# Optimization experiments

Measured on AMD Instinct MI355X. Metric: run time of the kernel, lower is better.

## Reference

```python
import jax, jax.numpy as jnp
import numpy as np
import math

# ---- module config (mirrors init_kwargs) ----
FRAME_H, FRAME_W = 480, 640
HFOV = 79.0
CAM_H_CM = 88.0            # camera_height * 100
NUM_SEM = 16
RES = 5                    # map_resolution (cm/cell)
MAP_SIZE_CM = 4800
DSC = 4                    # global_downscaling
DU = 4                     # du_scale
VR = 100                   # vision_range (cells)
CAT_THR, EXP_THR, MAP_THR = 5.0, 1.0, 1.0
MIN_D_CM, MAX_D_CM = 50.0, 350.0
NC = 6                     # MC.NON_SEM_CHANNELS
ML = MAP_SIZE_CM // DSC // RES   # 240 local map cells
MG = MAP_SIZE_CM // RES          # 960 global map cells
ZMIN = int(-40 / RES)            # -8
ZB = int(360 / RES) - ZMIN       # 80 z bins
MIN_MAP_H = int(25 / RES - ZMIN)            # 13
MAX_MAP_H = int((CAM_H_CM + 1) / RES - ZMIN)  # 25
BC_R = 200 // RES                # been-close radius (cells)
CENTER_POSE = (ML * RES) / 200.0 # agent start at local map center (m)


def _affine_grid(theta, H, W):
    # theta: (B,2,3); align_corners=True convention
    ys = jnp.linspace(-1.0, 1.0, H)
    xs = jnp.linspace(-1.0, 1.0, W)
    xg, yg = jnp.meshgrid(xs, ys)
    base = jnp.stack([xg, yg, jnp.ones_like(xg)], -1)  # (H,W,3)
    return jnp.einsum('bij,hwj->bhwi', theta, base)    # (B,H,W,2)


def _grid_sample(img, grid):
    # bilinear, align_corners=True, zero padding (matches F.grid_sample)
    B, C, H, W = img.shape
    x = (grid[..., 0] + 1.0) * 0.5 * (W - 1)
    y = (grid[..., 1] + 1.0) * 0.5 * (H - 1)
    x0, y0 = jnp.floor(x), jnp.floor(y)
    flat = img.reshape(B, C, H * W)
    out = jnp.zeros_like(img)
    for dx in (0.0, 1.0):
        for dy in (0.0, 1.0):
            xi, yi = x0 + dx, y0 + dy
            w = (1.0 - jnp.abs(x - xi)) * (1.0 - jnp.abs(y - yi))
            ok = (xi >= 0) & (xi <= W - 1) & (yi >= 0) & (yi <= H - 1)
            idx = (jnp.clip(yi, 0, H - 1).astype(jnp.int32) * W
                   + jnp.clip(xi, 0, W - 1).astype(jnp.int32))
            g = jnp.take_along_axis(flat, jnp.broadcast_to(idx.reshape(B, 1, -1), (B, C, H * W)), axis=2)
            out = out + g.reshape(B, C, H, W) * (w * ok)[:, None]
    return out


def _splat(gx, gy, gz, feat, valid):
    # trilinear scatter-add of per-point features into (VR,VR,ZB) voxel grid
    # gx,gy,gz,valid: (B,P); feat: (B,P,F)
    B, P = gx.shape
    F = feat.shape[-1]
    ncell = VR * VR * ZB
    acc = jnp.zeros((B * ncell, F), feat.dtype)
    base = (jnp.arange(B) * ncell)[:, None]
    x0, y0, z0 = jnp.floor(gx), jnp.floor(gy), jnp.floor(gz)
    for dx in (0.0, 1.0):
        for dy in (0.0, 1.0):
            for dz in (0.0, 1.0):
                xi, yi, zi = x0 + dx, y0 + dy, z0 + dz
                w = (1.0 - jnp.abs(gx - xi)) * (1.0 - jnp.abs(gy - yi)) * (1.0 - jnp.abs(gz - zi))
                ok = valid & (xi >= 0) & (xi < VR) & (yi >= 0) & (yi < VR) & (zi >= 0) & (zi < ZB)
                cell = (yi.astype(jnp.int32) * VR + xi.astype(jnp.int32)) * ZB + zi.astype(jnp.int32)
                idx = jnp.clip(base + cell, 0, B * ncell - 1).reshape(-1)
                upd = (feat * (w * ok.astype(feat.dtype))[..., None]).reshape(B * P, F)
                acc = acc.at[idx].add(upd)
    return acc.reshape(B, VR, VR, ZB, F).transpose(0, 4, 1, 2, 3)  # (B,F,VR,VR,ZB)


def _forward(seq_obs, seq_pose_delta, seq_camera_poses, init_local_map,
             init_global_map, init_local_pose, init_global_pose,
             init_lmb, init_origins, seq_dones, seq_update_global):
    B, T = seq_obs.shape[:2]
    C = NUM_SEM
    f = FRAME_W / (2.0 * math.tan(math.radians(HFOV) / 2.0))
    cx, cy = FRAME_W / 2.0, FRAME_H / 2.0
    xs = ((jnp.arange(0, FRAME_W, DU) - cx) / f).astype(jnp.float32)   # (Ws,)
    zr = ((cy - jnp.arange(0, FRAME_H, DU)) / f).astype(jnp.float32)   # (Hs,)
    # camera tilt (elevation) from extrinsics (identity -> 0)
    elev = jnp.arctan2(seq_camera_poses[:, 2, 1], seq_camera_poses[:, 2, 2])
    ce, se = jnp.cos(elev)[:, None, None], jnp.sin(elev)[:, None, None]
    Hs, Ws = FRAME_H // DU, FRAME_W // DU
    P = Hs * Ws
    row = jnp.arange(ML, dtype=jnp.float32)

    def step(carry, inp):
        local_map, global_map, pose = carry
        obs, pd, done, upd = inp
        done = done.astype(bool)
        upd = upd.astype(bool)
        # episode reset
        local_map = jnp.where(done[:, None, None, None], 0.0, local_map)
        global_map = jnp.where(done[:, None, None, None], 0.0, global_map)
        pose = jnp.where(done[:, None], jnp.array([CENTER_POSE, CENTER_POSE, 0.0], jnp.float32), pose)
        # pose update (get_new_pose_batch, degrees)
        tr = jnp.radians(pose[:, 2])
        nx = pose[:, 0] + pd[:, 0] * jnp.cos(tr) - pd[:, 1] * jnp.sin(tr)
        ny = pose[:, 1] + pd[:, 0] * jnp.sin(tr) + pd[:, 1] * jnp.cos(tr)
        nt = jnp.mod(pose[:, 2] + jnp.degrees(pd[:, 2]) + 180.0, 360.0) - 180.0
        pose = jnp.stack([nx, ny, nt], -1)
        # ---- depth -> egocentric point cloud (cm) ----
        d = obs[:, 3, ::DU, ::DU]                           # (B,Hs,Ws)
        valid = (d >= MIN_D_CM) & (d <= MAX_D_CM)
        lat = d * xs[None, None, :]
        up = d * zr[None, :, None]
        fwd = d * ce + up * se
        hgt = -d * se + up * ce + CAM_H_CM
        gx = (lat / RES + VR / 2.0).reshape(B, P)
        gy = (fwd / RES).reshape(B, P)
        gz = (hgt / RES - ZMIN).reshape(B, P)
        # features: occupancy + avg-pooled semantics (du_scale pooling)
        sem = obs[:, 4:].reshape(B, C, Hs, DU, Ws, DU).mean((3, 5))
        feat = jnp.concatenate([jnp.ones((B, 1, Hs, Ws), obs.dtype), sem], 1)
        feat = feat.reshape(B, 1 + C, P).transpose(0, 2, 1)  # (B,P,F)
        vox = _splat(gx, gy, gz, feat, valid.reshape(B, P))  # (B,F,VR,VR,ZB)
        agent_hp = vox[..., MIN_MAP_H:MAX_MAP_H].sum(-1)
        all_hp = vox.sum(-1)
        fp_map = jnp.clip(agent_hp[:, 0:1] / MAP_THR, 0.0, 1.0)
        fp_exp = jnp.clip(all_hp[:, 0:1] / EXP_THR, 0.0, 1.0)
        sem_pred = jnp.clip(agent_hp[:, 1:] / CAT_THR, 0.0, 1.0)
        agent_view = jnp.zeros((B, NC + C, ML, ML), obs.dtype)
        y1, x1 = ML // 2, ML // 2 - VR // 2
        agent_view = agent_view.at[:, 0:1, y1:y1 + VR, x1:x1 + VR].set(fp_map)
        agent_view = agent_view.at[:, 1:2, y1:y1 + VR, x1:x1 + VR].set(fp_exp)
        agent_view = agent_view.at[:, NC:, y1:y1 + VR, x1:x1 + VR].set(sem_pred)
        # ---- pose transform: rotation then translation grid_sample ----
        th = jnp.radians(90.0 - pose[:, 2])
        stx = -(pose[:, 0] * 100.0 / RES - ML / 2.0) / (ML / 2.0)
        sty = -(pose[:, 1] * 100.0 / RES - ML / 2.0) / (ML / 2.0)
        c, s = jnp.cos(th), jnp.sin(th)
        z0 = jnp.zeros_like(th)
        o1 = jnp.ones_like(th)
        th_rot = jnp.stack([jnp.stack([c, -s, z0], -1), jnp.stack([s, c, z0], -1)], 1)
        th_tr = jnp.stack([jnp.stack([o1, z0, stx], -1), jnp.stack([z0, o1, sty], -1)], 1)
        warped = _grid_sample(_grid_sample(agent_view, _affine_grid(th_rot, ML, ML)),
                              _affine_grid(th_tr, ML, ML))
        # dilate obstacle channel (3x3 ones kernel, 1 iter)
        obst = jax.lax.reduce_window(warped[:, 0:1], -jnp.inf, jax.lax.max,
                                     (1, 1, 3, 3), (1, 1, 1, 1), 'SAME')
        warped = warped.at[:, 0:1].set(obst)
        local_map = jnp.maximum(local_map, warped)
        # current location / visited / been-close disks
        acx, acy = pose[:, 0] * 100.0 / RES, pose[:, 1] * 100.0 / RES
        d2 = ((row[None, None, :] - acx[:, None, None]) ** 2
              + (row[None, :, None] - acy[:, None, None]) ** 2)
        curr = (d2 <= 4.0).astype(local_map.dtype)
        local_map = local_map.at[:, 2].set(curr)
        local_map = local_map.at[:, 3].max(curr)
        local_map = local_map.at[:, 4].max((d2 <= float(BC_R ** 2)).astype(local_map.dtype))
        # global map update at local map boundaries
        gnew = jax.vmap(lambda g, l, lm: jax.lax.dynamic_update_slice(g, l, (0, lm[0], lm[2])))(
            global_map, local_map, init_lmb)
        global_map = jnp.where(upd[:, None, None, None], gnew, global_map)
        gpose = pose + init_origins
        # map features: local NC ch + maxpooled global NC ch + local sem ch
        gmax = global_map[:, :NC].reshape(B, NC, MG // DSC, DSC, MG // DSC, DSC).max((3, 5))
        mf = jnp.concatenate([local_map[:, :NC], gmax, local_map[:, NC:]], 1)
        return (local_map, global_map, pose), (mf, pose, gpose)

    xs_t = (jnp.swapaxes(seq_obs, 0, 1), jnp.swapaxes(seq_pose_delta, 0, 1),
            jnp.swapaxes(seq_dones, 0, 1), jnp.swapaxes(seq_update_global, 0, 1))
    (fl, fg, _), (mfs, lps, gps) = jax.lax.scan(
        step, (init_local_map, init_global_map, init_local_pose), xs_t)
    seq_mf = jnp.swapaxes(mfs, 0, 1)
    seq_lp = jnp.swapaxes(lps, 0, 1)
    seq_gp = jnp.swapaxes(gps, 0, 1)
    seq_lmb = jnp.broadcast_to(init_lmb[:, None], (B, T, 4))
    seq_org = jnp.broadcast_to(init_origins[:, None], (B, T, 3))
    return seq_mf, fl, fg, seq_lp, seq_gp, seq_lmb, seq_org


def setup_inputs():
    key = jax.random.key(0)
    k0, k1 = jax.random.split(key)
    B, T = 4, 4
    obs = jax.random.uniform(k0, (B, T, 4 + NUM_SEM, FRAME_H, FRAME_W), jnp.float32)
    obs = obs.at[:, :, 3].set(MIN_D_CM + obs[:, :, 3] * (MAX_D_CM - MIN_D_CM))  # depth in cm
    obs = obs.at[:, :, 4:].set((obs[:, :, 4:] > 0.9).astype(jnp.float32))       # binary seg masks
    pd = jax.random.normal(k1, (B, T, 3), jnp.float32) * jnp.array([0.25, 0.05, 0.1], jnp.float32)
    lo = (MG - ML) // 2
    lmb = jnp.tile(jnp.array([[lo, lo + ML, lo, lo + ML]], jnp.int32), (B, 1))
    origins = jnp.concatenate([jnp.full((B, 2), lo * RES / 100.0, jnp.float32),
                               jnp.zeros((B, 1), jnp.float32)], 1)
    lp = jnp.concatenate([jnp.full((B, 2), CENTER_POSE, jnp.float32),
                          jnp.zeros((B, 1), jnp.float32)], 1)
    return {
        "seq_obs": obs,
        "seq_pose_delta": pd,
        "seq_camera_poses": jnp.broadcast_to(jnp.eye(4, dtype=jnp.float32), (B, 4, 4)),
        "init_local_map": jnp.zeros((B, NC + NUM_SEM, ML, ML), jnp.float32),
        "init_global_map": jnp.zeros((B, NC + NUM_SEM, MG, MG), jnp.float32),
        "init_local_pose": lp,
        "init_global_pose": lp + origins,
        "init_origins": origins,
        "seq_dones": jnp.zeros((B, T), jnp.int32),
        "seq_update_global": jnp.ones((B, T), jnp.int32),
        "init_lmb": lmb,
    }


def reference(seq_obs, seq_pose_delta, seq_camera_poses, init_local_map, init_global_map,
              init_local_pose, init_global_pose, init_origins, seq_dones,
              seq_update_global, init_lmb):
    return _forward(seq_obs, seq_pose_delta, seq_camera_poses, init_local_map,
                    init_global_map, init_local_pose, init_global_pose,
                    init_lmb, init_origins, seq_dones, seq_update_global)
```

## Files before the change

kernel.cpp:

```cpp
#include <hip/hip_runtime.h>
#include <math.h>

#ifndef M_PI
#define M_PI 3.14159265358979323846
#endif

#define BB 4
#define TT 4
#define NSEM 16
#define CHL 22
#define CHMF 28
#define ML 240
#define MG 960
#define VR 100
#define HS 120
#define WSW 160
#define NPL 18
#define CPAD 24
#define MLSQ (ML*ML)
#define MGSQ (MG*MG)
#define VRSQ (VR*VR)
#define PPT (HS*WSW)
#define NPART 12
#define PR 9
#define NGRP 5
#define NSPLAT (BB*TT*NPART*NGRP)

#define SZ_MF (BB*TT*CHMF*MLSQ)
#define SZ_FL (BB*CHL*MLSQ)
#define SZ_FG (BB*CHL*MGSQ)
#define OFF_FL SZ_MF
#define OFF_FG (OFF_FL + SZ_FL)
#define OFF_LP (OFF_FG + SZ_FG)
#define OFF_GP (OFF_LP + BB*TT*3)
#define OFF_LMB (OFF_GP + BB*TT*3)
#define OFF_ORG (OFF_LMB + BB*TT*4)

#define WS_SCAL 0
#define WS_FLAGS (WS_SCAL + BB*TT*8)
#define WS_CACHE (WS_FLAGS + 4*BB)
#define WS_PLANES (WS_CACHE + BB*6*MLSQ)
#define WS_I2 (WS_PLANES + BB*TT*VRSQ*CPAD)
#define PTSN (BB*TT*PPT)
#define WS_GY (WS_I2 + BB*TT*NPL*MLSQ)
#define WS_GX (WS_GY + PTSN)
#define WS_WZA (WS_GX + PTSN)
#define WS_WZL (WS_WZA + PTSN)
#define WS_SEMDS (WS_WZL + PTSN)

__device__ __forceinline__ void fginit_block(const float* __restrict__ igm,
                                             const int* __restrict__ dones,
                                             const int* __restrict__ updg,
                                             const int* __restrict__ lmb,
                                             float* __restrict__ fg,
                                             float* __restrict__ out,
                                             float* __restrict__ ws,
                                             int b, int c, int idx)
{
    int i = idx / ML, j = idx % ML;
    int lastDone = -1, lastUpd = -1;
    #pragma unroll
    for (int t = 0; t < TT; t++) {
        if (dones[b*TT+t]) lastDone = t;
        if (updg[b*TT+t])  lastUpd  = t;
    }
    bool anyDone = lastDone >= 0;
    bool zeroWin = lastUpd < lastDone;
    int y0 = lmb[b*4+0], x0 = lmb[b*4+2];
    int iy0 = y0 >> 2, ix0 = x0 >> 2;
    bool inWin = (i >= iy0) && (i < iy0 + ML/4) && (j >= ix0) && (j < ix0 + ML/4);

    size_t base = ((size_t)b*CHL + c)*MGSQ + (size_t)(4*i)*MG + 4*j;
    const float* g = igm + base;
    float* go = fg + base;

    int act;
    if (inWin) act = zeroWin ? 1 : ((lastUpd >= 0) ? 2 : (anyDone ? 1 : 0));
    else       act = anyDone ? 1 : 0;

    if (c < 6) {
        float m = -3.0e38f;
        #pragma unroll
        for (int r = 0; r < 4; r++) {
            float4 q = *(const float4*)(g + (size_t)r*MG);
            if (act == 0) *(float4*)(go + (size_t)r*MG) = q;
            else if (act == 1) *(float4*)(go + (size_t)r*MG) = make_float4(0,0,0,0);
            m = fmaxf(m, fmaxf(fmaxf(q.x, q.y), fmaxf(q.z, q.w)));
        }
        ws[WS_CACHE + ((size_t)b*6 + c)*MLSQ + idx] = m;
        if (!inWin) {
            float v = m;
            for (int t = 0; t < TT; t++) {
                if (dones[b*TT+t]) v = 0.0f;
                out[(size_t)(b*TT+t)*CHMF*MLSQ + (6+c)*MLSQ + idx] = v;
            }
        }
    } else {
        if (act == 2) return;
        if (act == 1) {
            float4 z = make_float4(0,0,0,0);
            #pragma unroll
            for (int r = 0; r < 4; r++) *(float4*)(go + (size_t)r*MG) = z;
        } else {
            #pragma unroll
            for (int r = 0; r < 4; r++)
                *(float4*)(go + (size_t)r*MG) = *(const float4*)(g + (size_t)r*MG);
        }
    }
}

__global__ __launch_bounds__(256) void k_node1(const float* __restrict__ obs,
                                               const float* __restrict__ cam,
                                               const float* __restrict__ pd,
                                               const float* __restrict__ ilp,
                                               const float* __restrict__ org,
                                               const int* __restrict__ lmb,
                                               const int* __restrict__ dones,
                                               const int* __restrict__ updg,
                                               const float* __restrict__ igm,
                                               float* __restrict__ fg,
                                               float* __restrict__ out,
                                               float* __restrict__ ws)
{
    if (blockIdx.x == 0) {
        int i = threadIdx.x;
        if (i < BB*TT) {
            int b = i / TT, t = i % TT;
            for (int k = 0; k < 4; k++) out[OFF_LMB + (b*TT+t)*4 + k] = (float)lmb[b*4+k];
            for (int k = 0; k < 3; k++) out[OFF_ORG + (b*TT+t)*3 + k] = org[b*3+k];
        }
        if (i >= BB) return;
        int b = i;
        float p0 = ilp[b*3+0], p1 = ilp[b*3+1], p2 = ilp[b*3+2];
        const float D2R = 0.017453292519943295f;
        int lastDone = -1, lastUpd = -1;
        for (int t = 0; t < TT; t++) {
            if (dones[b*TT+t]) { p0 = 6.0f; p1 = 6.0f; p2 = 0.0f; lastDone = t; }
            if (updg[b*TT+t]) lastUpd = t;
            float tr = p2 * D2R;
            float c0 = cosf(tr), s0 = sinf(tr);
            float q0 = pd[(b*TT+t)*3+0], q1 = pd[(b*TT+t)*3+1], q2 = pd[(b*TT+t)*3+2];
            float nx = p0 + q0*c0 - q1*s0;
            float ny = p1 + q0*s0 + q1*c0;
            float a  = p2 + q2*57.29577951308232f + 180.0f;
            float m  = fmodf(a, 360.0f); if (m < 0.0f) m += 360.0f;
            float nt = m - 180.0f;
            p0 = nx; p1 = ny; p2 = nt;
            out[OFF_LP + (b*TT+t)*3+0] = nx;
            out[OFF_LP + (b*TT+t)*3+1] = ny;
            out[OFF_LP + (b*TT+t)*3+2] = nt;
            out[OFF_GP + (b*TT+t)*3+0] = nx + org[b*3+0];
            out[OFF_GP + (b*TT+t)*3+1] = ny + org[b*3+1];
            out[OFF_GP + (b*TT+t)*3+2] = nt + org[b*3+2];
            float th = (90.0f - nt) * D2R;
            float ax = nx*100.0f/5.0f, ay = ny*100.0f/5.0f;
            float* sc = ws + WS_SCAL + (b*TT+t)*8;
            sc[0] = cosf(th);
            sc[1] = sinf(th);
            sc[2] = -(ax - 120.0f)/120.0f;
            sc[3] = -(ay - 120.0f)/120.0f;
            sc[4] = ax;
            sc[5] = ay;
        }
        ws[WS_FLAGS + b*4 + 0] = (lastDone >= 0) ? 1.0f : 0.0f;
        ws[WS_FLAGS + b*4 + 1] = (lastUpd < lastDone) ? 1.0f : 0.0f;
        ws[WS_FLAGS + b*4 + 2] = (float)lastUpd;
        return;
    }
    if (blockIdx.x <= 75*BB*TT) {
        int bb = blockIdx.x - 1;
        int bt = bb / 75;
        int b = bt / TT;
        int p = (bb % 75)*256 + threadIdx.x;
        int h = p / WSW, w = p % WSW;
        size_t pi = (size_t)bt*PPT + p;
        const float* ob = obs + (size_t)bt * 20 * 480 * 640;
        float d = ob[(size_t)(3*480 + 4*h)*640 + 4*w];
        if (!(d >= 50.0f && d <= 350.0f)) { ws[WS_GY + pi] = -1000.0f; return; }

        double fd = 640.0 / (2.0 * tan((79.0 * M_PI / 180.0) * 0.5));
        float ff  = (float)fd;
        float xsv = (float)(4*w - 320) / ff;
        float zrv = (240.0f - (float)(4*h)) / ff;
        float elev = atan2f(cam[b*16+9], cam[b*16+10]);
        float ce = cosf(elev), se = sinf(elev);
        float up  = d * zrv;
        float fwd = d*ce + up*se;
        float hgt = -d*se + up*ce + 88.0f;
        float gx = (d*xsv)/5.0f + 50.0f;
        float gy = fwd/5.0f;
        float gz = hgt/5.0f + 8.0f;

        float z0 = floorf(gz);
        float wza = 0.0f, wzl = 0.0f;
        #pragma unroll
        for (int dz = 0; dz < 2; dz++) {
            float zi = z0 + dz;
            float wz = 1.0f - fabsf(gz - zi);
            if (zi >= 0.0f && zi < 80.0f) {
                wzl += wz;
                if (zi >= 13.0f && zi < 25.0f) wza += wz;
            }
        }
        if (wzl == 0.0f && wza == 0.0f) { ws[WS_GY + pi] = -1000.0f; return; }

        ws[WS_GY + pi]  = gy;
        ws[WS_GX + pi]  = gx;
        ws[WS_WZA + pi] = wza;
        ws[WS_WZL + pi] = wzl;

        if (wza > 0.0f) {
            const float* sb = ob + (size_t)4*480*640 + (size_t)(4*h)*640 + 4*w;
            float* so = ws + WS_SEMDS + (size_t)bt*NSEM*PPT + p;
            #pragma unroll
            for (int k = 0; k < NSEM; k++) {
                float s = 0.0f;
                #pragma unroll
                for (int r = 0; r < 4; r++) {
                    const float4 v = *(const float4*)(sb + (size_t)k*480*640 + r*640);
                    s += v.x + v.y + v.z + v.w;
                }
                so[(size_t)k*PPT] = s * 0.0625f;
            }
        }
        return;
    }
    int fb = blockIdx.x - (1 + 75*BB*TT);
    int idx = (fb % 225)*256 + threadIdx.x;
    int c = (fb / 225) % 6;
    int b = fb / (225*6);
    fginit_block(igm, dones, updg, lmb, fg, out, ws, b, c, idx);
}

__global__ __launch_bounds__(256) void k_node2(const float* __restrict__ igm,
                                               const int* __restrict__ dones,
                                               const int* __restrict__ updg,
                                               const int* __restrict__ lmb,
                                               float* __restrict__ planes,
                                               float* __restrict__ fg,
                                               float* __restrict__ out,
                                               float* __restrict__ ws)
{
    __shared__ float acc[4*PR*VR];
    int bid = blockIdx.x;
    if (bid < NSPLAT) {
        int bt = bid & 15;
        int part = (bid >> 4) % NPART;
        int grp = bid / (16*NPART);
        int rlo = part * PR;
        int c0  = (grp == 0) ? 0 : (2 + 4*(grp-1));
        int nch = (grp == 0) ? 2 : 4;
        for (int e = threadIdx.x; e < nch*PR*VR; e += 256) acc[e] = 0.0f;
        __syncthreads();

        const float* gyA  = ws + WS_GY  + (size_t)bt*PPT;
        const float* gxA  = ws + WS_GX  + (size_t)bt*PPT;
        const float* wzaA = ws + WS_WZA + (size_t)bt*PPT;
        const float* wzlA = ws + WS_WZL + (size_t)bt*PPT;
        const float* semA = ws + WS_SEMDS + (size_t)bt*NSEM*PPT + (size_t)(c0-2)*PPT;

        for (int p = threadIdx.x; p < PPT; p += 256) {
            float gy = gyA[p];
            float y0 = floorf(gy);
            if (y0 > (float)(rlo + PR - 1) || y0 + 1.0f < (float)rlo) continue;
            float wza = wzaA[p];
            if (grp != 0 && wza <= 0.0f) continue;
            float gx  = gxA[p];
            float x0 = floorf(gx);
            float sem[4];
            if (grp != 0) {
                #pragma unroll
                for (int k = 0; k < 4; k++) sem[k] = semA[(size_t)k*PPT + p];
            }
            float wzl = (grp == 0) ? wzlA[p] : 0.0f;
            #pragma unroll
            for (int dy = 0; dy < 2; dy++) {
                float yi = y0 + dy;
                if (!(yi >= 0.0f && yi < 100.0f)) continue;
                int r = (int)yi - rlo;
                if (r < 0 || r >= PR) continue;
                float wy = 1.0f - fabsf(gy - yi);
                #pragma unroll
                for (int dx = 0; dx < 2; dx++) {
                    float xi = x0 + dx;
                    if (!(xi >= 0.0f && xi < 100.0f)) continue;
                    float wxy = (1.0f - fabsf(gx - xi)) * wy;
                    if (wxy <= 0.0f) continue;
                    int cell = r*VR + (int)xi;
                    if (grp == 0) {
                        if (wza > 0.0f) atomicAdd(&acc[cell], wza*wxy);
                        if (wzl > 0.0f) atomicAdd(&acc[PR*VR + cell], wzl*wxy);
                    } else {
                        #pragma unroll
                        for (int k = 0; k < 4; k++) {
                            float sv = sem[k];
                            if (sv != 0.0f) atomicAdd(&acc[k*PR*VR + cell], sv*wza*wxy);
                        }
                    }
                }
            }
        }
        __syncthreads();

        int nrows = 100 - rlo; if (nrows > PR) nrows = PR;
        if (nrows <= 0) return;
        float* pl = planes + (size_t)bt*VRSQ*CPAD;
        for (int e = threadIdx.x; e < nch*nrows*VR; e += 256) {
            int c = e / (nrows*VR);
            int rc = e % (nrows*VR);
            int r = rc / VR, x = rc % VR;
            pl[(size_t)((rlo + r)*VR + x)*CPAD + (c0 + c)] = acc[c*PR*VR + r*VR + x];
        }
        return;
    }
    int fb = bid - NSPLAT;
    int idx = (fb % 225)*256 + threadIdx.x;
    int c = 6 + (fb / 225) % 8;
    int b = fb / (225*8);
    fginit_block(igm, dones, updg, lmb, fg, out, ws, b, c, idx);
}

__global__ __launch_bounds__(256) void k_node3(const float* __restrict__ planes,
                                               const float* __restrict__ igm,
                                               const int* __restrict__ dones,
                                               const int* __restrict__ updg,
                                               const int* __restrict__ lmb,
                                               float* __restrict__ I2,
                                               float* __restrict__ fg,
                                               float* __restrict__ out,
                                               float* __restrict__ ws)
{
    int bid = blockIdx.x;
    if (bid < 3600) {
        int bt = bid / 225;
        int idx = (bid % 225)*256 + threadIdx.x;
        int i = idx / ML, j = idx % ML;
        const float* sc = ws + WS_SCAL + bt*8;
        float c = sc[0], s = sc[1], stx = sc[2], sty = sc[3];
        float* o = I2 + (size_t)bt*NPL*MLSQ + idx;
        const float* pl = planes + (size_t)bt*VRSQ*CPAD;

        int   soff[16];
        float sw[16];
        float wsum = 0.0f;
        {
            float xg = (float)j * (float)(2.0/239.0) - 1.0f + stx;
            float yg = (float)i * (float)(2.0/239.0) - 1.0f + sty;
            float x = (xg + 1.0f)*0.5f*239.0f;
            float y = (yg + 1.0f)*0.5f*239.0f;
            float x0 = floorf(x), y0 = floorf(y);
            #pragma unroll
            for (int dy = 0; dy < 2; dy++) {
                float yi = y0 + dy;
                bool vy = (yi >= 0.0f && yi <= 239.0f);
                float wy = 1.0f - fabsf(y - yi);
                #pragma unroll
                for (int dx = 0; dx < 2; dx++) {
                    float xi = x0 + dx;
                    bool vx = (xi >= 0.0f && xi <= 239.0f);
                    float w2v = (vy && vx) ? (1.0f - fabsf(x - xi)) * wy : 0.0f;
                    int ci = (dy*2 + dx)*4;
                    float xg1 = (float)(int)xi * (float)(2.0/239.0) - 1.0f;
                    float yg1 = (float)(int)yi * (float)(2.0/239.0) - 1.0f;
                    float gxr = c*xg1 - s*yg1;
                    float gyr = s*xg1 + c*yg1;
                    float xx = (gxr + 1.0f)*0.5f*239.0f;
                    float yy = (gyr + 1.0f)*0.5f*239.0f;
                    float xx0 = floorf(xx), yy0 = floorf(yy);
                    #pragma unroll
                    for (int dy1 = 0; dy1 < 2; dy1++) {
                        float syi = yy0 + dy1;
                        bool v1y = (syi >= 120.0f && syi < 220.0f);
                        float wy1 = 1.0f - fabsf(yy - syi);
                        #pragma unroll
                        for (int dx1 = 0; dx1 < 2; dx1++) {
                            float sxi = xx0 + dx1;
                            bool v1 = v1y && (sxi >= 70.0f && sxi < 170.0f);
                            float w1v = v1 ? (1.0f - fabsf(xx - sxi)) * wy1 : 0.0f;
                            float wt = w2v * w1v;
                            soff[ci + dy1*2 + dx1] = v1 ? ((int)syi - 120)*VR + ((int)sxi - 70) : 0;
                            sw[ci + dy1*2 + dx1] = wt;
                            wsum += wt;
                        }
                    }
                }
            }
        }

        if (wsum <= 0.0f) {
            #pragma unroll
            for (int cc = 0; cc < NPL; cc++) o[(size_t)cc*MLSQ] = 0.0f;
            return;
        }
        float acc[NPL];
        #pragma unroll
        for (int cc = 0; cc < NPL; cc++) acc[cc] = 0.0f;
        #pragma unroll
        for (int k = 0; k < 16; k++) {
            float w = sw[k];
            if (w == 0.0f) continue;
            const float* pb = pl + (size_t)soff[k]*CPAD;
            float4 a0 = *(const float4*)(pb + 0);
            float4 a1 = *(const float4*)(pb + 4);
            float4 a2 = *(const float4*)(pb + 8);
            float4 a3 = *(const float4*)(pb + 12);
            float2 a4 = *(const float2*)(pb + 16);
            acc[0]  += fminf(a0.x, 1.0f) * w;
            acc[1]  += fminf(a0.y, 1.0f) * w;
            acc[2]  += fminf(a0.z / 5.0f, 1.0f) * w;
            acc[3]  += fminf(a0.w / 5.0f, 1.0f) * w;
            acc[4]  += fminf(a1.x / 5.0f, 1.0f) * w;
            acc[5]  += fminf(a1.y / 5.0f, 1.0f) * w;
            acc[6]  += fminf(a1.z / 5.0f, 1.0f) * w;
            acc[7]  += fminf(a1.w / 5.0f, 1.0f) * w;
            acc[8]  += fminf(a2.x / 5.0f, 1.0f) * w;
            acc[9]  += fminf(a2.y / 5.0f, 1.0f) * w;
            acc[10] += fminf(a2.z / 5.0f, 1.0f) * w;
            acc[11] += fminf(a2.w / 5.0f, 1.0f) * w;
            acc[12] += fminf(a3.x / 5.0f, 1.0f) * w;
            acc[13] += fminf(a3.y / 5.0f, 1.0f) * w;
            acc[14] += fminf(a3.z / 5.0f, 1.0f) * w;
            acc[15] += fminf(a3.w / 5.0f, 1.0f) * w;
            acc[16] += fminf(a4.x / 5.0f, 1.0f) * w;
            acc[17] += fminf(a4.y / 5.0f, 1.0f) * w;
        }
        #pragma unroll
        for (int cc = 0; cc < NPL; cc++) o[(size_t)cc*MLSQ] = acc[cc];
        return;
    }
    int fb = bid - 3600;
    int idx = (fb % 225)*256 + threadIdx.x;
    int c = 14 + (fb / 225) % 8;
    int b = fb / (225*8);
    fginit_block(igm, dones, updg, lmb, fg, out, ws, b, c, idx);
}

__global__ __launch_bounds__(256) void k_updl7(const float* __restrict__ I2,
                                               const float* __restrict__ ws,
                                               const float* __restrict__ ilm,
                                               const int* __restrict__ dones,
                                               const int* __restrict__ updg,
                                               const int* __restrict__ lmb,
                                               float* __restrict__ fl,
                                               float* __restrict__ fg,
                                               float* __restrict__ out)
{
    int bz = blockIdx.z;
    int b = bz / 7, g = bz % 7;
    int gi = blockIdx.y;
    int bx = blockIdx.x;
    int lane = threadIdx.x & 63, wv = threadIdx.x >> 6;
    int j0 = (bx < 3) ? bx*64 : 176;
    int j = j0 + lane;
    int i = gi*4 + wv;
    int idx = i*ML + j;

    int ncl, cl[4];
    switch (g) {
        case 0:  ncl = 1; cl[0] = 0; cl[1] = 0; cl[2] = 0; cl[3] = 0; break;
        case 1:  ncl = 3; cl[0] = 1; cl[1] = 2; cl[2] = 3; cl[3] = 0; break;
        case 2:  ncl = 2; cl[0] = 4; cl[1] = 5; cl[2] = 0; cl[3] = 0; break;
        default: ncl = 4; { int cc0 = 6 + (g-3)*4;
                 cl[0] = cc0; cl[1] = cc0+1; cl[2] = cc0+2; cl[3] = cc0+3; } break;
    }
    bool hasG = (g <= 2);

    __shared__ float red[4][3][16];

    const float* lmsrc = ilm + (size_t)b*CHL*MLSQ;
    float* lm = fl + (size_t)b*CHL*MLSQ;
    int y0 = lmb[b*4+0], x0 = lmb[b*4+2];
    bool zeroWin = ws[WS_FLAGS + b*4 + 1] > 0.5f;
    int lastUpd = (int)ws[WS_FLAGS + b*4 + 2];

    float S[4];
    #pragma unroll
    for (int q = 0; q < 4; q++) {
        int c = cl[q];
        S[q] = (q < ncl && c != 2) ? lmsrc[c*MLSQ + idx] : 0.0f;
    }

    bool writer = hasG && (wv == 0) && ((lane & 3) == 0);
    int cx = lane >> 2;
    int cellY = (y0 >> 2) + gi;
    int cellX = (x0 >> 2) + (j0 >> 2) + cx;
    float W[3];
    if (writer) {
        #pragma unroll
        for (int q = 0; q < 3; q++)
            if (q < ncl)
                W[q] = ws[WS_CACHE + ((size_t)b*6 + cl[q])*MLSQ + cellY*ML + cellX];
    }

    for (int t = 0; t < TT; t++) {
        int bt = b*TT + t;
        bool done = dones[bt] != 0;
        bool upd  = updg[bt] != 0;
        const float* src = I2 + (size_t)bt*NPL*MLSQ;
        float* mf = out + (size_t)bt*CHMF*MLSQ;

        float pooled = -3.0e38f;
        if (g == 0) {
            for (int di = -1; di <= 1; di++) {
                int ii = i + di; if (ii < 0 || ii >= ML) continue;
                for (int dj = -1; dj <= 1; dj++) {
                    int jj = j + dj; if (jj < 0 || jj >= ML) continue;
                    pooled = fmaxf(pooled, src[ii*ML + jj]);
                }
            }
        }
        const float* sc = ws + WS_SCAL + bt*8;
        float acx = sc[4], acy = sc[5];
        float ddx = (float)j - acx, ddy = (float)i - acy;
        float d2 = ddx*ddx + ddy*ddy;
        float curr = (d2 <= 4.0f) ? 1.0f : 0.0f;
        float bc   = (d2 <= 1600.0f) ? 1.0f : 0.0f;

        size_t goff = (size_t)(y0+i)*MG + (x0+j);
        bool wrG = (t == lastUpd) && !zeroWin;

        #pragma unroll
        for (int q = 0; q < 4; q++) {
            if (q >= ncl) continue;
            int c = cl[q];
            if (done) S[q] = 0.0f;
            float nv;
            if      (c == 0) nv = fmaxf(S[q], pooled);
            else if (c == 1) nv = fmaxf(S[q], src[MLSQ + idx]);
            else if (c == 2) nv = curr;
            else if (c == 3) nv = fmaxf(S[q], curr);
            else if (c == 4) nv = fmaxf(S[q], bc);
            else if (c == 5) nv = S[q];
            else             nv = fmaxf(S[q], src[(size_t)(c-4)*MLSQ + idx]);
            S[q] = nv;
            mf[(size_t)(c < 6 ? c : c + 6)*MLSQ + idx] = nv;
            if (wrG) fg[((size_t)b*CHL + c)*MGSQ + goff] = nv;
        }

        if (hasG) {
            #pragma unroll
            for (int q = 0; q < 3; q++) {
                if (q >= ncl) continue;
                float v = S[q];
                v = fmaxf(v, __shfl_xor(v, 1, 64));
                v = fmaxf(v, __shfl_xor(v, 2, 64));
                if ((lane & 3) == 0) red[wv][q][cx] = v;
            }
            __syncthreads();
            if (writer) {
                #pragma unroll
                for (int q = 0; q < 3; q++) {
                    if (q >= ncl) continue;
                    if (done) W[q] = 0.0f;
                    if (upd)  W[q] = fmaxf(fmaxf(red[0][q][cx], red[1][q][cx]),
                                           fmaxf(red[2][q][cx], red[3][q][cx]));
                    mf[(size_t)(6 + cl[q])*MLSQ + cellY*ML + cellX] = W[q];
                }
            }
            __syncthreads();
        }
    }
    #pragma unroll
    for (int q = 0; q < 4; q++)
        if (q < ncl) lm[(size_t)cl[q]*MLSQ + idx] = S[q];
}

extern "C" void kernel_launch(void* const* d_in, const int* in_sizes, int n_in,
                              void* d_out, int out_size, void* d_ws, size_t ws_size,
                              hipStream_t stream)
{
    const float* obs   = (const float*)d_in[0];
    const float* pd    = (const float*)d_in[1];
    const float* cam   = (const float*)d_in[2];
    const float* ilm   = (const float*)d_in[3];
    const float* igm   = (const float*)d_in[4];
    const float* ilp   = (const float*)d_in[5];
    const float* org   = (const float*)d_in[7];
    const int*   dones = (const int*)d_in[8];
    const int*   updg  = (const int*)d_in[9];
    const int*   lmb   = (const int*)d_in[10];
    float* out = (float*)d_out;
    float* ws  = (float*)d_ws;

    float* fl     = out + OFF_FL;
    float* fg     = out + OFF_FG;
    float* planes = ws + WS_PLANES;
    float* I2v    = ws + WS_I2;

    k_node1<<<1 + 75*BB*TT + 225*6*BB, 256, 0, stream>>>(obs, cam, pd, ilp, org, lmb,
                                                         dones, updg, igm, fg, out, ws);
    k_node2<<<NSPLAT + 225*8*BB, 256, 0, stream>>>(igm, dones, updg, lmb,
                                                   planes, fg, out, ws);
    k_node3<<<3600 + 225*8*BB, 256, 0, stream>>>(planes, igm, dones, updg, lmb,
                                                 I2v, fg, out, ws);
    k_updl7<<<dim3(4, 60, BB*7), 256, 0, stream>>>(I2v, ws, ilm, dones, updg, lmb,
                                                   fl, fg, out);
}
```

Baseline: 370.4 us.

## Move global-map init work out of splat and sample kernels into final update kernel

Separates the voxel splat and grid-sample stages into dedicated kernels that no longer carry trailing global-map initialisation blocks. The initialisation of channels 6–21 of the global map is instead appended to the final local/global update kernel, which now uses a flattened 1D grid. The aim is to keep the latency-sensitive splat and sample stages free of bandwidth-heavy filler blocks and to overlap that copy with the final update. The risk is that the last kernel becomes larger and memory-bound, so the same traffic may simply move rather than hide.

```diff
diff --git a/kernel.cpp b/kernel.cpp
--- a/kernel.cpp
+++ b/kernel.cpp
@@ -25,6 +25,7 @@
 #define PR 9
 #define NGRP 5
 #define NSPLAT (BB*TT*NPART*NGRP)
+#define NUPDL (4*60*BB*7)
 
 #define SZ_MF (BB*TT*CHMF*MLSQ)
 #define SZ_FL (BB*CHL*MLSQ)
@@ -232,210 +233,182 @@
     fginit_block(igm, dones, updg, lmb, fg, out, ws, b, c, idx);
 }
 
-__global__ __launch_bounds__(256) void k_node2(const float* __restrict__ igm,
-                                               const int* __restrict__ dones,
-                                               const int* __restrict__ updg,
-                                               const int* __restrict__ lmb,
-                                               float* __restrict__ planes,
-                                               float* __restrict__ fg,
-                                               float* __restrict__ out,
-                                               float* __restrict__ ws)
+__global__ __launch_bounds__(256) void k_splat2(const float* __restrict__ ws,
+                                                float* __restrict__ planes)
 {
     __shared__ float acc[4*PR*VR];
     int bid = blockIdx.x;
-    if (bid < NSPLAT) {
-        int bt = bid & 15;
-        int part = (bid >> 4) % NPART;
-        int grp = bid / (16*NPART);
-        int rlo = part * PR;
-        int c0  = (grp == 0) ? 0 : (2 + 4*(grp-1));
-        int nch = (grp == 0) ? 2 : 4;
-        for (int e = threadIdx.x; e < nch*PR*VR; e += 256) acc[e] = 0.0f;
-        __syncthreads();
-
-        const float* gyA  = ws + WS_GY  + (size_t)bt*PPT;
-        const float* gxA  = ws + WS_GX  + (size_t)bt*PPT;
-        const float* wzaA = ws + WS_WZA + (size_t)bt*PPT;
-        const float* wzlA = ws + WS_WZL + (size_t)bt*PPT;
-        const float* semA = ws + WS_SEMDS + (size_t)bt*NSEM*PPT + (size_t)(c0-2)*PPT;
-
-        for (int p = threadIdx.x; p < PPT; p += 256) {
-            float gy = gyA[p];
-            float y0 = floorf(gy);
-            if (y0 > (float)(rlo + PR - 1) || y0 + 1.0f < (float)rlo) continue;
-            float wza = wzaA[p];
-            if (grp != 0 && wza <= 0.0f) continue;
-            float gx  = gxA[p];
-            float x0 = floorf(gx);
-            float sem[4];
-            if (grp != 0) {
-                #pragma unroll
-                for (int k = 0; k < 4; k++) sem[k] = semA[(size_t)k*PPT + p];
-            }
-            float wzl = (grp == 0) ? wzlA[p] : 0.0f;
-            #pragma unroll
-            for (int dy = 0; dy < 2; dy++) {
-                float yi = y0 + dy;
-                if (!(yi >= 0.0f && yi < 100.0f)) continue;
-                int r = (int)yi - rlo;
-                if (r < 0 || r >= PR) continue;
-                float wy = 1.0f - fabsf(gy - yi);
-                #pragma unroll
-                for (int dx = 0; dx < 2; dx++) {
-                    float xi = x0 + dx;
-                    if (!(xi >= 0.0f && xi < 100.0f)) continue;
-                    float wxy = (1.0f - fabsf(gx - xi)) * wy;
-                    if (wxy <= 0.0f) continue;
-                    int cell = r*VR + (int)xi;
-                    if (grp == 0) {
-                        if (wza > 0.0f) atomicAdd(&acc[cell], wza*wxy);
-                        if (wzl > 0.0f) atomicAdd(&acc[PR*VR + cell], wzl*wxy);
-                    } else {
-                        #pragma unroll
-                        for (int k = 0; k < 4; k++) {
-                            float sv = sem[k];
-                            if (sv != 0.0f) atomicAdd(&acc[k*PR*VR + cell], sv*wza*wxy);
-                        }
+    int bt = bid & 15;
+    int part = (bid >> 4) % NPART;
+    int grp = bid / (16*NPART);
+    int rlo = part * PR;
+    int c0  = (grp == 0) ? 0 : (2 + 4*(grp-1));
+    int nch = (grp == 0) ? 2 : 4;
+    for (int e = threadIdx.x; e < nch*PR*VR; e += 256) acc[e] = 0.0f;
+    __syncthreads();
+
+    const float* gyA  = ws + WS_GY  + (size_t)bt*PPT;
+    const float* gxA  = ws + WS_GX  + (size_t)bt*PPT;
+    const float* wzaA = ws + WS_WZA + (size_t)bt*PPT;
+    const float* wzlA = ws + WS_WZL + (size_t)bt*PPT;
+    const float* semA = ws + WS_SEMDS + (size_t)bt*NSEM*PPT + (size_t)(c0-2)*PPT;
+
+    for (int p = threadIdx.x; p < PPT; p += 256) {
+        float gy = gyA[p];
+        float y0 = floorf(gy);
+        if (y0 > (float)(rlo + PR - 1) || y0 + 1.0f < (float)rlo) continue;
+        float wza = wzaA[p];
+        if (grp != 0 && wza <= 0.0f) continue;
+        float gx  = gxA[p];
+        float x0 = floorf(gx);
+        float sem[4];
+        if (grp != 0) {
+            #pragma unroll
+            for (int k = 0; k < 4; k++) sem[k] = semA[(size_t)k*PPT + p];
+        }
+        float wzl = (grp == 0) ? wzlA[p] : 0.0f;
+        #pragma unroll
+        for (int dy = 0; dy < 2; dy++) {
+            float yi = y0 + dy;
+            if (!(yi >= 0.0f && yi < 100.0f)) continue;
+            int r = (int)yi - rlo;
+            if (r < 0 || r >= PR) continue;
+            float wy = 1.0f - fabsf(gy - yi);
+            #pragma unroll
+            for (int dx = 0; dx < 2; dx++) {
+                float xi = x0 + dx;
+                if (!(xi >= 0.0f && xi < 100.0f)) continue;
+                float wxy = (1.0f - fabsf(gx - xi)) * wy;
+                if (wxy <= 0.0f) continue;
+                int cell = r*VR + (int)xi;
+                if (grp == 0) {
+                    if (wza > 0.0f) atomicAdd(&acc[cell], wza*wxy);
+                    if (wzl > 0.0f) atomicAdd(&acc[PR*VR + cell], wzl*wxy);
+                } else {
+                    #pragma unroll
+                    for (int k = 0; k < 4; k++) {
+                        float sv = sem[k];
+                        if (sv != 0.0f) atomicAdd(&acc[k*PR*VR + cell], sv*wza*wxy);
                     }
                 }
             }
         }
-        __syncthreads();
-
-        int nrows = 100 - rlo; if (nrows > PR) nrows = PR;
-        if (nrows <= 0) return;
-        float* pl = planes + (size_t)bt*VRSQ*CPAD;
-        for (int e = threadIdx.x; e < nch*nrows*VR; e += 256) {
-            int c = e / (nrows*VR);
-            int rc = e % (nrows*VR);
-            int r = rc / VR, x = rc % VR;
-            pl[(size_t)((rlo + r)*VR + x)*CPAD + (c0 + c)] = acc[c*PR*VR + r*VR + x];
-        }
-        return;
-    }
-    int fb = bid - NSPLAT;
-    int idx = (fb % 225)*256 + threadIdx.x;
-    int c = 6 + (fb / 225) % 8;
-    int b = fb / (225*8);
-    fginit_block(igm, dones, updg, lmb, fg, out, ws, b, c, idx);
+    }
+    __syncthreads();
+
+    int nrows = 100 - rlo; if (nrows > PR) nrows = PR;
+    if (nrows <= 0) return;
+    float* pl = planes + (size_t)bt*VRSQ*CPAD;
+    for (int e = threadIdx.x; e < nch*nrows*VR; e += 256) {
+        int c = e / (nrows*VR);
+        int rc = e % (nrows*VR);
+        int r = rc / VR, x = rc % VR;
+        pl[(size_t)((rlo + r)*VR + x)*CPAD + (c0 + c)] = acc[c*PR*VR + r*VR + x];
+    }
 }
 
-__global__ __launch_bounds__(256) void k_node3(const float* __restrict__ planes,
-                                               const float* __restrict__ igm,
-                                               const int* __restrict__ dones,
-                                               const int* __restrict__ updg,
-                                               const int* __restrict__ lmb,
-                                               float* __restrict__ I2,
-                                               float* __restrict__ fg,
-                                               float* __restrict__ out,
-                                               float* __restrict__ ws)
+__global__ __launch_bounds__(256) void k_gs(const float* __restrict__ planes,
+                                            const float* __restrict__ ws,
+                                            float* __restrict__ I2)
 {
-    int bid = blockIdx.x;
-    if (bid < 3600) {
-        int bt = bid / 225;
-        int idx = (bid % 225)*256 + threadIdx.x;
-        int i = idx / ML, j = idx % ML;
-        const float* sc = ws + WS_SCAL + bt*8;
-        float c = sc[0], s = sc[1], stx = sc[2], sty = sc[3];
-        float* o = I2 + (size_t)bt*NPL*MLSQ + idx;
-        const float* pl = planes + (size_t)bt*VRSQ*CPAD;
-
-        int   soff[16];
-        float sw[16];
-        float wsum = 0.0f;
-        {
-            float xg = (float)j * (float)(2.0/239.0) - 1.0f + stx;
-            float yg = (float)i * (float)(2.0/239.0) - 1.0f + sty;
-            float x = (xg + 1.0f)*0.5f*239.0f;
-            float y = (yg + 1.0f)*0.5f*239.0f;
-            float x0 = floorf(x), y0 = floorf(y);
-            #pragma unroll
-            for (int dy = 0; dy < 2; dy++) {
-                float yi = y0 + dy;
-                bool vy = (yi >= 0.0f && yi <= 239.0f);
-                float wy = 1.0f - fabsf(y - yi);
+    int bt = blockIdx.x / 225;
+    int idx = (blockIdx.x % 225)*256 + threadIdx.x;
+    int i = idx / ML, j = idx % ML;
+    const float* sc = ws + WS_SCAL + bt*8;
+    float c = sc[0], s = sc[1], stx = sc[2], sty = sc[3];
+    float* o = I2 + (size_t)bt*NPL*MLSQ + idx;
+    const float* pl = planes + (size_t)bt*VRSQ*CPAD;
+
+    int   soff[16];
+    float sw[16];
+    float wsum = 0.0f;
+    {
+        float xg = (float)j * (float)(2.0/239.0) - 1.0f + stx;
+        float yg = (float)i * (float)(2.0/239.0) - 1.0f + sty;
+        float x = (xg + 1.0f)*0.5f*239.0f;
+        float y = (yg + 1.0f)*0.5f*239.0f;
+        float x0 = floorf(x), y0 = floorf(y);
+        #pragma unroll
+        for (int dy = 0; dy < 2; dy++) {
+            float yi = y0 + dy;
+            bool vy = (yi >= 0.0f && yi <= 239.0f);
+            float wy = 1.0f - fabsf(y - yi);
+            #pragma unroll
+            for (int dx = 0; dx < 2; dx++) {
+                float xi = x0 + dx;
+                bool vx = (xi >= 0.0f && xi <= 239.0f);
+                float w2v = (vy && vx) ? (1.0f - fabsf(x - xi)) * wy : 0.0f;
+                int ci = (dy*2 + dx)*4;
+                float xg1 = (float)(int)xi * (float)(2.0/239.0) - 1.0f;
+                float yg1 = (float)(int)yi * (float)(2.0/239.0) - 1.0f;
+                float gxr = c*xg1 - s*yg1;
+                float gyr = s*xg1 + c*yg1;
+                float xx = (gxr + 1.0f)*0.5f*239.0f;
+                float yy = (gyr + 1.0f)*0.5f*239.0f;
+                float xx0 = floorf(xx), yy0 = floorf(yy);
                 #pragma unroll
-                for (int dx = 0; dx < 2; dx++) {
-                    float xi = x0 + dx;
-                    bool vx = (xi >= 0.0f && xi <= 239.0f);
-                    float w2v = (vy && vx) ? (1.0f - fabsf(x - xi)) * wy : 0.0f;
-                    int ci = (dy*2 + dx)*4;
-                    float xg1 = (float)(int)xi * (float)(2.0/239.0) - 1.0f;
-                    float yg1 = (float)(int)yi * (float)(2.0/239.0) - 1.0f;
-                    float gxr = c*xg1 - s*yg1;
-                    float gyr = s*xg1 + c*yg1;
-                    float xx = (gxr + 1.0f)*0.5f*239.0f;
-                    float yy = (gyr + 1.0f)*0.5f*239.0f;
-                    float xx0 = floorf(xx), yy0 = floorf(yy);
+                for (int dy1 = 0; dy1 < 2; dy1++) {
+                    float syi = yy0 + dy1;
+                    bool v1y = (syi >= 120.0f && syi < 220.0f);
+                    float wy1 = 1.0f - fabsf(yy - syi);
                     #pragma unroll
-                    for (int dy1 = 0; dy1 < 2; dy1++) {
-                        float syi = yy0 + dy1;
-                        bool v1y = (syi >= 120.0f && syi < 220.0f);
-                        float wy1 = 1.0f - fabsf(yy - syi);
-                        #pragma unroll
-                        for (int dx1 = 0; dx1 < 2; dx1++) {
-                            float sxi = xx0 + dx1;
-                            bool v1 = v1y && (sxi >= 70.0f && sxi < 170.0f);
-                            float w1v = v1 ? (1.0f - fabsf(xx - sxi)) * wy1 : 0.0f;
-                            float wt = w2v * w1v;
-                            soff[ci + dy1*2 + dx1] = v1 ? ((int)syi - 120)*VR + ((int)sxi - 70) : 0;
-                            sw[ci + dy1*2 + dx1] = wt;
-                            wsum += wt;
-                        }
+                    for (int dx1 = 0; dx1 < 2; dx1++) {
+                        float sxi = xx0 + dx1;
+                        bool v1 = v1y && (sxi >= 70.0f && sxi < 170.0f);
+                        float w1v = v1 ? (1.0f - fabsf(xx - sxi)) * wy1 : 0.0f;
+                        float wt = w2v * w1v;
+                        soff[ci + dy1*2 + dx1] = v1 ? ((int)syi - 120)*VR + ((int)sxi - 70) : 0;
+                        sw[ci + dy1*2 + dx1] = wt;
+                        wsum += wt;
                     }
                 }
             }
         }
-
-        if (wsum <= 0.0f) {
-            #pragma unroll
-            for (int cc = 0; cc < NPL; cc++) o[(size_t)cc*MLSQ] = 0.0f;
-            return;
-        }
-        float acc[NPL];
-        #pragma unroll
-        for (int cc = 0; cc < NPL; cc++) acc[cc] = 0.0f;
-        #pragma unroll
-        for (int k = 0; k < 16; k++) {
-            float w = sw[k];
-            if (w == 0.0f) continue;
-            const float* pb = pl + (size_t)soff[k]*CPAD;
-            float4 a0 = *(const float4*)(pb + 0);
-            float4 a1 = *(const float4*)(pb + 4);
-            float4 a2 = *(const float4*)(pb + 8);
-            float4 a3 = *(const float4*)(pb + 12);
-            float2 a4 = *(const float2*)(pb + 16);
-            acc[0]  += fminf(a0.x, 1.0f) * w;
-            acc[1]  += fminf(a0.y, 1.0f) * w;
-            acc[2]  += fminf(a0.z / 5.0f, 1.0f) * w;
-            acc[3]  += fminf(a0.w / 5.0f, 1.0f) * w;
-            acc[4]  += fminf(a1.x / 5.0f, 1.0f) * w;
-            acc[5]  += fminf(a1.y / 5.0f, 1.0f) * w;
-            acc[6]  += fminf(a1.z / 5.0f, 1.0f) * w;
-            acc[7]  += fminf(a1.w / 5.0f, 1.0f) * w;
-            acc[8]  += fminf(a2.x / 5.0f, 1.0f) * w;
-            acc[9]  += fminf(a2.y / 5.0f, 1.0f) * w;
-            acc[10] += fminf(a2.z / 5.0f, 1.0f) * w;
-            acc[11] += fminf(a2.w / 5.0f, 1.0f) * w;
-            acc[12] += fminf(a3.x / 5.0f, 1.0f) * w;
-            acc[13] += fminf(a3.y / 5.0f, 1.0f) * w;
-            acc[14] += fminf(a3.z / 5.0f, 1.0f) * w;
-            acc[15] += fminf(a3.w / 5.0f, 1.0f) * w;
-            acc[16] += fminf(a4.x / 5.0f, 1.0f) * w;
-            acc[17] += fminf(a4.y / 5.0f, 1.0f) * w;
-        }
-        #pragma unroll
-        for (int cc = 0; cc < NPL; cc++) o[(size_t)cc*MLSQ] = acc[cc];
+    }
+
+    if (wsum <= 0.0f) {
+        #pragma unroll
+        for (int cc = 0; cc < NPL; cc++) o[(size_t)cc*MLSQ] = 0.0f;
         return;
     }
-    int fb = bid - 3600;
-    int idx = (fb % 225)*256 + threadIdx.x;
-    int c = 14 + (fb / 225) % 8;
-    int b = fb / (225*8);
-    fginit_block(igm, dones, updg, lmb, fg, out, ws, b, c, idx);
+    float acc[NPL];
+    #pragma unroll
+    for (int cc = 0; cc < NPL; cc++) acc[cc] = 0.0f;
+    #pragma unroll
+    for (int k = 0; k < 16; k++) {
+        float w = sw[k];
+        if (w == 0.0f) continue;
+        const float* pb = pl + (size_t)soff[k]*CPAD;
+        float4 a0 = *(const float4*)(pb + 0);
+        float4 a1 = *(const float4*)(pb + 4);
+        float4 a2 = *(const float4*)(pb + 8);
+        float4 a3 = *(const float4*)(pb + 12);
+        float2 a4 = *(const float2*)(pb + 16);
+        acc[0]  += fminf(a0.x, 1.0f) * w;
+        acc[1]  += fminf(a0.y, 1.0f) * w;
+        acc[2]  += fminf(a0.z / 5.0f, 1.0f) * w;
+        acc[3]  += fminf(a0.w / 5.0f, 1.0f) * w;
+        acc[4]  += fminf(a1.x / 5.0f, 1.0f) * w;
+        acc[5]  += fminf(a1.y / 5.0f, 1.0f) * w;
+        acc[6]  += fminf(a1.z / 5.0f, 1.0f) * w;
+        acc[7]  += fminf(a1.w / 5.0f, 1.0f) * w;
+        acc[8]  += fminf(a2.x / 5.0f, 1.0f) * w;
+        acc[9]  += fminf(a2.y / 5.0f, 1.0f) * w;
+        acc[10] += fminf(a2.z / 5.0f, 1.0f) * w;
+        acc[11] += fminf(a2.w / 5.0f, 1.0f) * w;
+        acc[12] += fminf(a3.x / 5.0f, 1.0f) * w;
+        acc[13] += fminf(a3.y / 5.0f, 1.0f) * w;
+        acc[14] += fminf(a3.z / 5.0f, 1.0f) * w;
+        acc[15] += fminf(a3.w / 5.0f, 1.0f) * w;
+        acc[16] += fminf(a4.x / 5.0f, 1.0f) * w;
+        acc[17] += fminf(a4.y / 5.0f, 1.0f) * w;
+    }
+    #pragma unroll
+    for (int cc = 0; cc < NPL; cc++) o[(size_t)cc*MLSQ] = acc[cc];
 }
 
-__global__ __launch_bounds__(256) void k_updl7(const float* __restrict__ I2,
+__global__ __launch_bounds__(256) void k_node4(const float* __restrict__ I2,
+                                               const float* __restrict__ igm,
                                                const float* __restrict__ ws,
                                                const float* __restrict__ ilm,
                                                const int* __restrict__ dones,
@@ -443,12 +416,23 @@
                                                const int* __restrict__ lmb,
                                                float* __restrict__ fl,
                                                float* __restrict__ fg,
-                                               float* __restrict__ out)
+                                               float* __restrict__ out,
+                                               float* __restrict__ wsm)
 {
-    int bz = blockIdx.z;
+    __shared__ float red[4][3][16];
+    int bid = blockIdx.x;
+    if (bid >= NUPDL) {
+        int fb = bid - NUPDL;
+        int idx = (fb % 225)*256 + threadIdx.x;
+        int c = 6 + (fb / 225) % 16;
+        int b = fb / (225*16);
+        fginit_block(igm, dones, updg, lmb, fg, out, wsm, b, c, idx);
+        return;
+    }
+    int bx = bid & 3;
+    int gi = (bid >> 2) % 60;
+    int bz = bid / 240;
     int b = bz / 7, g = bz % 7;
-    int gi = blockIdx.y;
-    int bx = blockIdx.x;
     int lane = threadIdx.x & 63, wv = threadIdx.x >> 6;
     int j0 = (bx < 3) ? bx*64 : 176;
     int j = j0 + lane;
@@ -465,13 +449,11 @@
     }
     bool hasG = (g <= 2);
 
-    __shared__ float red[4][3][16];
-
     const float* lmsrc = ilm + (size_t)b*CHL*MLSQ;
     float* lm = fl + (size_t)b*CHL*MLSQ;
     int y0 = lmb[b*4+0], x0 = lmb[b*4+2];
-    bool zeroWin = ws[WS_FLAGS + b*4 + 1] > 0.5f;
-    int lastUpd = (int)ws[WS_FLAGS + b*4 + 2];
+    bool zeroWin = wsm[WS_FLAGS + b*4 + 1] > 0.5f;
+    int lastUpd = (int)wsm[WS_FLAGS + b*4 + 2];
 
     float S[4];
     #pragma unroll
@@ -489,7 +471,7 @@
         #pragma unroll
         for (int q = 0; q < 3; q++)
             if (q < ncl)
-                W[q] = ws[WS_CACHE + ((size_t)b*6 + cl[q])*MLSQ + cellY*ML + cellX];
+                W[q] = wsm[WS_CACHE + ((size_t)b*6 + cl[q])*MLSQ + cellY*ML + cellX];
     }
 
     for (int t = 0; t < TT; t++) {
@@ -509,7 +491,7 @@
                 }
             }
         }
-        const float* sc = ws + WS_SCAL + bt*8;
+        const float* sc = wsm + WS_SCAL + bt*8;
         float acx = sc[4], acy = sc[5];
         float ddx = (float)j - acx, ddy = (float)i - acy;
         float d2 = ddx*ddx + ddy*ddy;
@@ -589,10 +571,8 @@
 
     k_node1<<<1 + 75*BB*TT + 225*6*BB, 256, 0, stream>>>(obs, cam, pd, ilp, org, lmb,
                                                          dones, updg, igm, fg, out, ws);
-    k_node2<<<NSPLAT + 225*8*BB, 256, 0, stream>>>(igm, dones, updg, lmb,
-                                                   planes, fg, out, ws);
-    k_node3<<<3600 + 225*8*BB, 256, 0, stream>>>(planes, igm, dones, updg, lmb,
-                                                 I2v, fg, out, ws);
-    k_updl7<<<dim3(4, 60, BB*7), 256, 0, stream>>>(I2v, ws, ilm, dones, updg, lmb,
-                                                   fl, fg, out);
+    k_splat2<<<NSPLAT, 256, 0, stream>>>(ws, planes);
+    k_gs<<<3600, 256, 0, stream>>>(planes, ws, I2v);
+    k_node4<<<NUPDL + 225*16*BB, 256, 0, stream>>>(I2v, igm, ws, ilm, dones, updg, lmb,
+                                                   fl, fg, out, ws);
 }
```

After: 381.1 us. +2.9%, slower.
